# Performance work log

Hardware: AMD Instinct MI355X
Metric: run time of the kernel (lower is better)

Reference implementation:

```python
import jax, jax.numpy as jnp
import numpy as np

ROPE_DIM = 64       # config.rope_dim
GN_GROUPS = 32      # config.group_norm_num
GN_CHANNELS = 2048  # config.group_norm_channels == intermediate_size
GN_EPS = 1e-5


def rope_rotate(x):
    """lucidrains rotary-embedding-torch rotate_queries_or_keys:
    interleaved-pair rotation of the first ROPE_DIM features, rest pass through."""
    T = x.shape[-2]
    inv_freq = 1.0 / (10000.0 ** (jnp.arange(0, ROPE_DIM, 2, dtype=jnp.float32) / ROPE_DIM))
    freqs = jnp.arange(T, dtype=jnp.float32)[:, None] * inv_freq[None, :]  # (T, ROPE_DIM/2)
    freqs = jnp.repeat(freqs, 2, axis=-1)                                  # (T, ROPE_DIM)
    cos, sin = jnp.cos(freqs), jnp.sin(freqs)
    xr = x[..., :ROPE_DIM]
    x1, x2 = xr[..., 0::2], xr[..., 1::2]
    rot = jnp.stack((-x2, x1), axis=-1).reshape(xr.shape)  # rotate_half, interleaved
    xr = xr * cos + rot * sin
    return jnp.concatenate([xr, x[..., ROPE_DIM:]], axis=-1)


def group_norm_rows(x2d, weight, bias):
    """torch GroupNorm on a 2D (N, C) input: normalize each group of channels per row."""
    N, Cc = x2d.shape
    xg = x2d.reshape(N, GN_GROUPS, Cc // GN_GROUPS)
    mu = xg.mean(-1, keepdims=True)
    var = xg.var(-1, keepdims=True)
    xn = ((xg - mu) * jax.lax.rsqrt(var + GN_EPS)).reshape(N, Cc)
    return xn * weight + bias


def setup_inputs() -> dict:
    key = jax.random.key(0)
    ks = jax.random.split(key, 4)
    B, T, I, C = 2, 4096, 2048, 2048
    X = jax.random.normal(ks[0], (B, T, I), dtype=jnp.float32)
    S_n = jnp.zeros((B, C), dtype=jnp.float32)
    W_Q = jax.random.normal(ks[1], (I, C), dtype=jnp.float32) / I
    hh_b = jax.random.normal(ks[2], (C,), dtype=jnp.float32) * 0.02  # nn.Linear bias of self.hh
    gn_weight = jnp.ones((C,), dtype=jnp.float32)
    gn_bias = jnp.zeros((C,), dtype=jnp.float32)
    return {"X": X, "S_n": S_n, "W_Q": W_Q, "hh_b": hh_b,
            "gn_weight": gn_weight, "gn_bias": gn_bias}


def reference(X, S_n, W_Q, hh_b, gn_weight, gn_bias):
    # forward_auto_rec with chunk_len = T (single chunk, h_t starts at zeros):
    #   Q = ReLU(rope(X @ W_Q));  H = tanh(hh(0) + Q) = tanh(Q + b_hh)
    # K, V and the decay-masked A = (H K^T * D) V are computed in the source but
    # discarded (out = H), so they are dead code (DCE'd under jit) and omitted.
    B, T, _ = X.shape
    Q = jax.nn.relu(rope_rotate(X @ W_Q))   # (B, T, C)
    H = jnp.tanh(Q + hh_b)                  # (B, T, C)
    C = H.shape[-1]
    # dropout in eval mode = identity
    out = group_norm_rows(H.reshape(-1, C), gn_weight, gn_bias).reshape(B, T, C)
    # out.transpose(-2,-1).contiguous().view(B,T,C): reshape of the transposed layout
    out = jnp.swapaxes(out, -2, -1).reshape(B, T, C)
    return out, S_n
```

## Files before the change

kernel.cpp:

```cpp
#include <hip/hip_runtime.h>

#define T_DIM 4096
#define C_DIM 2048
#define K_DIM 2048

typedef __bf16 bf16x8 __attribute__((ext_vector_type(8)));
typedef float f32x4 __attribute__((ext_vector_type(4)));

__device__ __forceinline__ unsigned short f2bf(float f) {
  union { float f; unsigned int i; } x;
  x.f = f;
  unsigned int r = x.i + 0x7fffu + ((x.i >> 16) & 1u);
  return (unsigned short)(r >> 16);
}

#define GLD16(gsrc, ldst)                                                   \
  __builtin_amdgcn_global_load_lds(                                         \
      (const __attribute__((address_space(1))) unsigned int*)(gsrc),        \
      (__attribute__((address_space(3))) unsigned int*)(ldst), 16, 0, 0)

__global__ __launch_bounds__(256) void transpose_w(const float* __restrict__ W,
                                                   unsigned short* __restrict__ Wt) {
  __shared__ float tile[64][68];
  const int c0 = blockIdx.x * 64;
  const int r0 = blockIdx.y * 64;
  const int tid = threadIdx.x;
#pragma unroll
  for (int i = 0; i < 4; ++i) {
    int s = tid + i * 256;
    int r = s >> 4, c4 = (s & 15) * 4;
    *(float4*)&tile[r][c4] = *(const float4*)&W[(size_t)(r0 + r) * C_DIM + c0 + c4];
  }
  __syncthreads();
#pragma unroll
  for (int i = 0; i < 2; ++i) {
    int s = tid + i * 256;
    int n = s >> 3, k8 = (s & 7) * 8;
    __align__(16) unsigned short tmp[8];
#pragma unroll
    for (int j = 0; j < 8; ++j) tmp[j] = f2bf(tile[k8 + j][n]);
    *(uint4*)&Wt[(size_t)(c0 + n) * K_DIM + r0 + k8] = *(uint4*)tmp;
  }
}

__global__ __launch_bounds__(256) void cvt_x(const float* __restrict__ X,
                                             unsigned short* __restrict__ Xb) {
  size_t base = (size_t)blockIdx.x * 2048 + (size_t)threadIdx.x * 8;
  float4 a = *(const float4*)&X[base];
  float4 b = *(const float4*)&X[base + 4];
  __align__(16) unsigned short t[8];
  t[0] = f2bf(a.x); t[1] = f2bf(a.y); t[2] = f2bf(a.z); t[3] = f2bf(a.w);
  t[4] = f2bf(b.x); t[5] = f2bf(b.y); t[6] = f2bf(b.z); t[7] = f2bf(b.w);
  *(uint4*)&Xb[base] = *(const uint4*)t;
}

#define FOR_MN(OP) \
  OP(0,0) OP(0,1) OP(0,2) OP(0,3) \
  OP(1,0) OP(1,1) OP(1,2) OP(1,3) \
  OP(2,0) OP(2,1) OP(2,2) OP(2,3) \
  OP(3,0) OP(3,1) OP(3,2) OP(3,3)

#define DECL_ACC(m,n) f32x4 a##m##n = {0.f, 0.f, 0.f, 0.f};

template <bool ABF16>
__global__ __launch_bounds__(256, 2) void gemm_fused(const void* __restrict__ Av,
                                                     const unsigned short* __restrict__ Wt,
                                                     const float* __restrict__ hhb,
                                                     const float* __restrict__ gnw,
                                                     const float* __restrict__ gnb,
                                                     float* __restrict__ out) {
  constexpr int SMEM_BYTES = ABF16 ? 65536 : 49152;
  __shared__ __align__(16) char smem[SMEM_BYTES];
  unsigned short* lsA = (unsigned short*)smem;
  float* lsAf = (float*)smem;
  unsigned short* lsB = (unsigned short*)(smem + 32768);
  float(*lsO)[68] = (float(*)[68])smem;

  const int tid = threadIdx.x;
  const int wave = tid >> 6;
  const int lane = tid & 63;
  const int quad = lane >> 4;
  const int l16 = lane & 15;
  const int wm = wave >> 1, wn = wave & 1;

  const int bid = blockIdx.x;
  const int wg = (bid & 7) * 128 + (bid >> 3);
  const int m0 = (wg >> 4) * 128;
  const int n0 = (wg & 15) * 128;

  FOR_MN(DECL_ACC)

  if constexpr (ABF16) {
    const int srow = lane >> 3;
    const int scol = ((lane & 7) ^ (srow & 7)) * 8;
    const unsigned short* gA =
        (const unsigned short*)Av + (size_t)(m0 + wave * 32 + srow) * K_DIM + scol;
    const unsigned short* gB =
        Wt + (size_t)(n0 + wave * 32 + srow) * K_DIM + scol;

    const int xs0 = (quad * 8) ^ ((l16 & 7) << 3);
    const int xs1 = (32 + quad * 8) ^ ((l16 & 7) << 3);
    const int abase = (wm * 64 + l16) * 64;
    const int bbase = (wn * 64 + l16) * 64;

    auto stage = [&](int d, int koff) {
#pragma unroll
      for (int r = 0; r < 4; ++r)
        GLD16(gA + (size_t)(r * 8) * K_DIM + koff, lsA + d * 8192 + wave * 2048 + r * 512);
#pragma unroll
      for (int r = 0; r < 4; ++r)
        GLD16(gB + (size_t)(r * 8) * K_DIM + koff, lsB + d * 8192 + wave * 2048 + r * 512);
    };

    constexpr int NT = K_DIM / 64;
    stage(0, 0);
    for (int t = 0; t < NT; ++t) {
      const int cur = t & 1;
      if (t + 1 < NT) {
        stage(cur ^ 1, (t + 1) * 64);
        asm volatile("s_waitcnt vmcnt(8)" ::: "memory");
      } else {
        asm volatile("s_waitcnt vmcnt(0)" ::: "memory");
      }
      __builtin_amdgcn_s_barrier();
      asm volatile("" ::: "memory");

      const unsigned short* pa = lsA + cur * 8192;
      const unsigned short* pb = lsB + cur * 8192;

#define LOAD_AF16(m, XS) bf16x8 af##m = *(const bf16x8*)(const void*)(pa + abase + m * 1024 + XS);
#define LOAD_BF16(n, XS) bf16x8 bfr##n = *(const bf16x8*)(const void*)(pb + bbase + n * 1024 + XS);
#define MFMA_OP(m,n) \
      a##m##n = __builtin_amdgcn_mfma_f32_16x16x32_bf16(af##m, bfr##n, a##m##n, 0, 0, 0);
      {
        LOAD_AF16(0, xs0) LOAD_AF16(1, xs0) LOAD_AF16(2, xs0) LOAD_AF16(3, xs0)
        LOAD_BF16(0, xs0) LOAD_BF16(1, xs0) LOAD_BF16(2, xs0) LOAD_BF16(3, xs0)
        FOR_MN(MFMA_OP)
      }
      {
        LOAD_AF16(0, xs1) LOAD_AF16(1, xs1) LOAD_AF16(2, xs1) LOAD_AF16(3, xs1)
        LOAD_BF16(0, xs1) LOAD_BF16(1, xs1) LOAD_BF16(2, xs1) LOAD_BF16(3, xs1)
        FOR_MN(MFMA_OP)
      }
#undef LOAD_AF16
#undef LOAD_BF16

      asm volatile("s_waitcnt lgkmcnt(0)" ::: "memory");
      __builtin_amdgcn_sched_barrier(0);
      __builtin_amdgcn_s_barrier();
      asm volatile("" ::: "memory");
    }
  } else {
    const int srow32 = lane >> 3;
    const int scol32 = (((lane & 7) ^ srow32) * 4);
    const int srow16 = lane >> 2;
    const int scol16 = (((lane & 3) ^ (srow16 & 3)) * 8);
    const float* gA32 =
        (const float*)Av + (size_t)(m0 + wave * 32 + srow32) * K_DIM + scol32;
    const unsigned short* gB16 =
        Wt + (size_t)(n0 + wave * 32 + srow16) * K_DIM + scol16;

    const int axs = (quad ^ (l16 & 3)) * 8;
    const int bbase = (wn * 64 + l16) * 32 + axs;
    const int abasef = (wm * 64 + l16) * 32;
    const int u0 = ((2 * quad) ^ (l16 & 7)) * 4;
    const int u1 = ((2 * quad + 1) ^ (l16 & 7)) * 4;

    auto stage = [&](int d, int koff) {
      GLD16(gA32 + koff, lsAf + d * 4096 + wave * 1024);
      GLD16(gA32 + koff + 8 * K_DIM, lsAf + d * 4096 + wave * 1024 + 256);
      GLD16(gA32 + koff + 16 * K_DIM, lsAf + d * 4096 + wave * 1024 + 512);
      GLD16(gA32 + koff + 24 * K_DIM, lsAf + d * 4096 + wave * 1024 + 768);
      GLD16(gB16 + koff, lsB + d * 4096 + wave * 1024);
      GLD16(gB16 + koff + 16 * K_DIM, lsB + d * 4096 + wave * 1024 + 512);
    };

    constexpr int NT = K_DIM / 32;
    stage(0, 0);
    for (int t = 0; t < NT; ++t) {
      const int cur = t & 1;
      if (t + 1 < NT) {
        stage(cur ^ 1, (t + 1) * 32);
        asm volatile("s_waitcnt vmcnt(6)" ::: "memory");
      } else {
        asm volatile("s_waitcnt vmcnt(0)" ::: "memory");
      }
      __builtin_amdgcn_s_barrier();
      asm volatile("" ::: "memory");

      const float* paf = lsAf + cur * 4096;
      const unsigned short* pb = lsB + cur * 4096;

#define LOAD_AF32(m)                                                      \
      bf16x8 af##m;                                                       \
      { const float* ap_ = paf + abasef + m * 512;                        \
        f32x4 a0_ = *(const f32x4*)(ap_ + u0);                            \
        f32x4 a1_ = *(const f32x4*)(ap_ + u1);                            \
        af##m[0] = (__bf16)a0_[0]; af##m[1] = (__bf16)a0_[1];             \
        af##m[2] = (__bf16)a0_[2]; af##m[3] = (__bf16)a0_[3];             \
        af##m[4] = (__bf16)a1_[0]; af##m[5] = (__bf16)a1_[1];             \
        af##m[6] = (__bf16)a1_[2]; af##m[7] = (__bf16)a1_[3]; }
#define LOAD_BF32(n)                                                      \
      bf16x8 bfr##n = *(const bf16x8*)(const void*)(pb + bbase + n * 512);

      LOAD_AF32(0) LOAD_AF32(1) LOAD_AF32(2) LOAD_AF32(3)
      LOAD_BF32(0) LOAD_BF32(1) LOAD_BF32(2) LOAD_BF32(3)
      FOR_MN(MFMA_OP)
#undef LOAD_AF32
#undef LOAD_BF32

      asm volatile("s_waitcnt lgkmcnt(0)" ::: "memory");
      __builtin_amdgcn_sched_barrier(0);
      __builtin_amdgcn_s_barrier();
      asm volatile("" ::: "memory");
    }
  }

  const int c_base = n0 + wn * 64;
  const int t_base = (m0 & (T_DIM - 1)) + wm * 64;

#define LOADC(n)                                  \
  const int c##n = c_base + n * 16 + l16;         \
  const float hb##n = hhb[c##n];                  \
  const float gw##n = gnw[c##n];                  \
  const float gb##n = gnb[c##n];
  LOADC(0) LOADC(1) LOADC(2) LOADC(3)

  if (c_base == 0) {
#define ROPE_E(n,m,r)                                                   \
    { float v_ = a##m##n[r];                                            \
      float p_ = __shfl_xor(v_, 1, 64);                                 \
      int t_ = t_base + m * 16 + quad * 4 + r;                          \
      float ang_ = (float)t_ * fr_;                                     \
      float s_ = sinf(ang_);                                            \
      float co_ = cosf(ang_);                                           \
      a##m##n[r] = v_ * co_ + sg_ * p_ * s_; }
#define ROPE_M(n,m) ROPE_E(n,m,0) ROPE_E(n,m,1) ROPE_E(n,m,2) ROPE_E(n,m,3)
#define ROPE_N(n)                                                       \
    { int cc_ = n * 16 + l16;                                           \
      int ii_ = cc_ >> 1;                                               \
      float fr_ = expf(-(float)ii_ * 0.28782313662425572f);             \
      float sg_ = (cc_ & 1) ? 1.f : -1.f;                               \
      ROPE_M(n,0) ROPE_M(n,1) ROPE_M(n,2) ROPE_M(n,3) }
    ROPE_N(0) ROPE_N(1) ROPE_N(2) ROPE_N(3)
  }

#define GN_ROW(m,r)                                                     \
  { float h0_ = tanhf(fmaxf(a##m##0[r], 0.f) + hb0);                    \
    float h1_ = tanhf(fmaxf(a##m##1[r], 0.f) + hb1);                    \
    float h2_ = tanhf(fmaxf(a##m##2[r], 0.f) + hb2);                    \
    float h3_ = tanhf(fmaxf(a##m##3[r], 0.f) + hb3);                    \
    float s1_ = h0_ + h1_ + h2_ + h3_;                                  \
    float s2_ = h0_ * h0_ + h1_ * h1_ + h2_ * h2_ + h3_ * h3_;          \
    s1_ += __shfl_xor(s1_, 1, 64);  s2_ += __shfl_xor(s2_, 1, 64);      \
    s1_ += __shfl_xor(s1_, 2, 64);  s2_ += __shfl_xor(s2_, 2, 64);      \
    s1_ += __shfl_xor(s1_, 4, 64);  s2_ += __shfl_xor(s2_, 4, 64);      \
    s1_ += __shfl_xor(s1_, 8, 64);  s2_ += __shfl_xor(s2_, 8, 64);      \
    float mu_ = s1_ * 0.015625f;                                        \
    float var_ = s2_ * 0.015625f - mu_ * mu_;                           \
    float rs_ = rsqrtf(var_ + 1e-5f);                                   \
    a##m##0[r] = (h0_ - mu_) * rs_ * gw0 + gb0;                         \
    a##m##1[r] = (h1_ - mu_) * rs_ * gw1 + gb1;                         \
    a##m##2[r] = (h2_ - mu_) * rs_ * gw2 + gb2;                         \
    a##m##3[r] = (h3_ - mu_) * rs_ * gw3 + gb3; }
#define GN_M(m) GN_ROW(m,0) GN_ROW(m,1) GN_ROW(m,2) GN_ROW(m,3)
  GN_M(0) GN_M(1) GN_M(2) GN_M(3)

  const int bb = m0 >> 12;
  const int t0 = m0 & (T_DIM - 1);
#define ST_MN(m,n)                                                      \
  lsO[wn * 64 + n * 16 + l16][m * 16 + quad * 4 + 0] = a##m##n[0];      \
  lsO[wn * 64 + n * 16 + l16][m * 16 + quad * 4 + 1] = a##m##n[1];      \
  lsO[wn * 64 + n * 16 + l16][m * 16 + quad * 4 + 2] = a##m##n[2];      \
  lsO[wn * 64 + n * 16 + l16][m * 16 + quad * 4 + 3] = a##m##n[3];
#pragma unroll
  for (int h = 0; h < 2; ++h) {
    if (wm == h) {
      FOR_MN(ST_MN)
    }
    __syncthreads();
#pragma unroll
    for (int i = 0; i < 8; ++i) {
      int s = tid + i * 256;
      int cl = s >> 4;
      int t4 = (s & 15) * 4;
      float4 v = *(const float4*)&lsO[cl][t4];
      *(float4*)&out[(size_t)bb * C_DIM * T_DIM + (size_t)(n0 + cl) * T_DIM + t0 + h * 64 + t4] = v;
    }
    __syncthreads();
  }
}

__global__ __launch_bounds__(256) void copy_sn(const float* __restrict__ src,
                                               float* __restrict__ dst) {
  int i = blockIdx.x * 256 + threadIdx.x;
  dst[i] = src[i];
}

extern "C" void kernel_launch(void* const* d_in, const int* in_sizes, int n_in,
                              void* d_out, int out_size, void* d_ws, size_t ws_size,
                              hipStream_t stream) {
  const float* X = (const float*)d_in[0];
  const float* Sn = (const float*)d_in[1];
  const float* W = (const float*)d_in[2];
  const float* hhb = (const float*)d_in[3];
  const float* gnw = (const float*)d_in[4];
  const float* gnb = (const float*)d_in[5];
  float* out = (float*)d_out;

  unsigned short* Wt = (unsigned short*)d_ws;
  const size_t wt_bytes = (size_t)C_DIM * K_DIM * 2;
  const size_t xb_bytes = (size_t)2 * T_DIM * K_DIM * 2;

  transpose_w<<<dim3(32, 32), dim3(256), 0, stream>>>(W, Wt);

  if (ws_size >= wt_bytes + xb_bytes) {
    unsigned short* Xb = Wt + (size_t)C_DIM * K_DIM;
    cvt_x<<<dim3(8192), dim3(256), 0, stream>>>(X, Xb);
    gemm_fused<true><<<dim3(1024), dim3(256), 0, stream>>>(Xb, Wt, hhb, gnw, gnb, out);
  } else {
    gemm_fused<false><<<dim3(1024), dim3(256), 0, stream>>>(X, Wt, hhb, gnw, gnb, out);
  }

  copy_sn<<<dim3(16), dim3(256), 0, stream>>>(Sn, out + (size_t)16777216);
}
```

Baseline: 295.6 us.

## Shrink bf16 GEMM K-tile to 32 and raise occupancy to four blocks per CU

The bf16-A GEMM path now stages 32-wide K tiles instead of 64-wide ones. This roughly halves its LDS footprint, and launch bounds are raised from 2 to 4 blocks per CU so more waves can hide latency. The LDS swizzle is changed to a new XOR pattern that avoids bank conflicts with 32-element rows, and the fp32-A path adopts the same B swizzle. In exchange there are twice as many barrier-synchronised iterations, each issuing fewer MFMAs, and the tighter register cap may cause spills.

```diff
diff --git a/kernel.cpp b/kernel.cpp
--- a/kernel.cpp
+++ b/kernel.cpp
@@ -62,18 +62,21 @@
 
 #define DECL_ACC(m,n) f32x4 a##m##n = {0.f, 0.f, 0.f, 0.f};
 
+#define MFMA_OP(m,n) \
+  a##m##n = __builtin_amdgcn_mfma_f32_16x16x32_bf16(af##m, bfr##n, a##m##n, 0, 0, 0);
+
 template <bool ABF16>
-__global__ __launch_bounds__(256, 2) void gemm_fused(const void* __restrict__ Av,
+__global__ __launch_bounds__(256, 4) void gemm_fused(const void* __restrict__ Av,
                                                      const unsigned short* __restrict__ Wt,
                                                      const float* __restrict__ hhb,
                                                      const float* __restrict__ gnw,
                                                      const float* __restrict__ gnb,
                                                      float* __restrict__ out) {
-  constexpr int SMEM_BYTES = ABF16 ? 65536 : 49152;
+  constexpr int SMEM_BYTES = ABF16 ? 34816 : 49152;
   __shared__ __align__(16) char smem[SMEM_BYTES];
   unsigned short* lsA = (unsigned short*)smem;
   float* lsAf = (float*)smem;
-  unsigned short* lsB = (unsigned short*)(smem + 32768);
+  unsigned short* lsB = (unsigned short*)(smem + (ABF16 ? 16384 : 32768));
   float(*lsO)[68] = (float(*)[68])smem;
 
   const int tid = threadIdx.x;
@@ -91,57 +94,45 @@
   FOR_MN(DECL_ACC)
 
   if constexpr (ABF16) {
-    const int srow = lane >> 3;
-    const int scol = ((lane & 7) ^ (srow & 7)) * 8;
+    const int srow = lane >> 2;
+    const int scol = ((lane & 3) ^ ((lane >> 3) & 3)) * 8;
     const unsigned short* gA =
         (const unsigned short*)Av + (size_t)(m0 + wave * 32 + srow) * K_DIM + scol;
     const unsigned short* gB =
         Wt + (size_t)(n0 + wave * 32 + srow) * K_DIM + scol;
 
-    const int xs0 = (quad * 8) ^ ((l16 & 7) << 3);
-    const int xs1 = (32 + quad * 8) ^ ((l16 & 7) << 3);
-    const int abase = (wm * 64 + l16) * 64;
-    const int bbase = (wn * 64 + l16) * 64;
+    const int axs = (quad ^ ((l16 >> 1) & 3)) * 8;
+    const int abase = (wm * 64 + l16) * 32;
+    const int bbase = (wn * 64 + l16) * 32;
 
     auto stage = [&](int d, int koff) {
-#pragma unroll
-      for (int r = 0; r < 4; ++r)
-        GLD16(gA + (size_t)(r * 8) * K_DIM + koff, lsA + d * 8192 + wave * 2048 + r * 512);
-#pragma unroll
-      for (int r = 0; r < 4; ++r)
-        GLD16(gB + (size_t)(r * 8) * K_DIM + koff, lsB + d * 8192 + wave * 2048 + r * 512);
+      GLD16(gA + koff, lsA + d * 4096 + wave * 1024);
+      GLD16(gA + (size_t)16 * K_DIM + koff, lsA + d * 4096 + wave * 1024 + 512);
+      GLD16(gB + koff, lsB + d * 4096 + wave * 1024);
+      GLD16(gB + (size_t)16 * K_DIM + koff, lsB + d * 4096 + wave * 1024 + 512);
     };
 
-    constexpr int NT = K_DIM / 64;
+    constexpr int NT = K_DIM / 32;
     stage(0, 0);
     for (int t = 0; t < NT; ++t) {
       const int cur = t & 1;
       if (t + 1 < NT) {
-        stage(cur ^ 1, (t + 1) * 64);
-        asm volatile("s_waitcnt vmcnt(8)" ::: "memory");
+        stage(cur ^ 1, (t + 1) * 32);
+        asm volatile("s_waitcnt vmcnt(4)" ::: "memory");
       } else {
         asm volatile("s_waitcnt vmcnt(0)" ::: "memory");
       }
       __builtin_amdgcn_s_barrier();
       asm volatile("" ::: "memory");
 
-      const unsigned short* pa = lsA + cur * 8192;
-      const unsigned short* pb = lsB + cur * 8192;
-
-#define LOAD_AF16(m, XS) bf16x8 af##m = *(const bf16x8*)(const void*)(pa + abase + m * 1024 + XS);
-#define LOAD_BF16(n, XS) bf16x8 bfr##n = *(const bf16x8*)(const void*)(pb + bbase + n * 1024 + XS);
-#define MFMA_OP(m,n) \
-      a##m##n = __builtin_amdgcn_mfma_f32_16x16x32_bf16(af##m, bfr##n, a##m##n, 0, 0, 0);
-      {
-        LOAD_AF16(0, xs0) LOAD_AF16(1, xs0) LOAD_AF16(2, xs0) LOAD_AF16(3, xs0)
-        LOAD_BF16(0, xs0) LOAD_BF16(1, xs0) LOAD_BF16(2, xs0) LOAD_BF16(3, xs0)
-        FOR_MN(MFMA_OP)
-      }
-      {
-        LOAD_AF16(0, xs1) LOAD_AF16(1, xs1) LOAD_AF16(2, xs1) LOAD_AF16(3, xs1)
-        LOAD_BF16(0, xs1) LOAD_BF16(1, xs1) LOAD_BF16(2, xs1) LOAD_BF16(3, xs1)
-        FOR_MN(MFMA_OP)
-      }
+      const unsigned short* pa = lsA + cur * 4096;
+      const unsigned short* pb = lsB + cur * 4096;
+
+#define LOAD_AF16(m) bf16x8 af##m = *(const bf16x8*)(const void*)(pa + abase + m * 512 + axs);
+#define LOAD_BF16(n) bf16x8 bfr##n = *(const bf16x8*)(const void*)(pb + bbase + n * 512 + axs);
+      LOAD_AF16(0) LOAD_AF16(1) LOAD_AF16(2) LOAD_AF16(3)
+      LOAD_BF16(0) LOAD_BF16(1) LOAD_BF16(2) LOAD_BF16(3)
+      FOR_MN(MFMA_OP)
 #undef LOAD_AF16
 #undef LOAD_BF16
 
@@ -154,14 +145,14 @@
     const int srow32 = lane >> 3;
     const int scol32 = (((lane & 7) ^ srow32) * 4);
     const int srow16 = lane >> 2;
-    const int scol16 = (((lane & 3) ^ (srow16 & 3)) * 8);
+    const int scol16 = ((lane & 3) ^ ((lane >> 3) & 3)) * 8;
     const float* gA32 =
         (const float*)Av + (size_t)(m0 + wave * 32 + srow32) * K_DIM + scol32;
     const unsigned short* gB16 =
         Wt + (size_t)(n0 + wave * 32 + srow16) * K_DIM + scol16;
 
-    const int axs = (quad ^ (l16 & 3)) * 8;
-    const int bbase = (wn * 64 + l16) * 32 + axs;
+    const int bxs = (quad ^ ((l16 >> 1) & 3)) * 8;
+    const int bbase = (wn * 64 + l16) * 32;
     const int abasef = (wm * 64 + l16) * 32;
     const int u0 = ((2 * quad) ^ (l16 & 7)) * 4;
     const int u1 = ((2 * quad + 1) ^ (l16 & 7)) * 4;
@@ -172,7 +163,7 @@
       GLD16(gA32 + koff + 16 * K_DIM, lsAf + d * 4096 + wave * 1024 + 512);
       GLD16(gA32 + koff + 24 * K_DIM, lsAf + d * 4096 + wave * 1024 + 768);
       GLD16(gB16 + koff, lsB + d * 4096 + wave * 1024);
-      GLD16(gB16 + koff + 16 * K_DIM, lsB + d * 4096 + wave * 1024 + 512);
+      GLD16(gB16 + (size_t)16 * K_DIM + koff, lsB + d * 4096 + wave * 1024 + 512);
     };
 
     constexpr int NT = K_DIM / 32;
@@ -201,7 +192,7 @@
         af##m[4] = (__bf16)a1_[0]; af##m[5] = (__bf16)a1_[1];             \
         af##m[6] = (__bf16)a1_[2]; af##m[7] = (__bf16)a1_[3]; }
 #define LOAD_BF32(n)                                                      \
-      bf16x8 bfr##n = *(const bf16x8*)(const void*)(pb + bbase + n * 512);
+      bf16x8 bfr##n = *(const bf16x8*)(const void*)(pb + bbase + n * 512 + bxs);
 
       LOAD_AF32(0) LOAD_AF32(1) LOAD_AF32(2) LOAD_AF32(3)
       LOAD_BF32(0) LOAD_BF32(1) LOAD_BF32(2) LOAD_BF32(3)
```

Measured after the change: 410.9 us. +39.0%, slower.

## Use 256x256 block tile with 8 waves for the bf16 fused GEMM path

Applied to the files above, without the earlier changes.

Replaces the 128x128 bf16 GEMM kernel with a 256x256 tile kernel that runs 512 threads in a 2x4 wave grid, each wave holding 8x4 MFMA accumulators. It uses 128KB of LDS for double buffering. The goal is to cut global and LDS traffic per FLOP and reach higher MFMA intensity, at the cost of fewer blocks (256), which is roughly one per CU, and much higher register pressure. The fp32 fallback kernel is split into its own function and gets a modified B-tile swizzle.

```diff
diff --git a/kernel.cpp b/kernel.cpp
--- a/kernel.cpp
+++ b/kernel.cpp
@@ -54,179 +54,15 @@
   *(uint4*)&Xb[base] = *(const uint4*)t;
 }
 
-#define FOR_MN(OP) \
-  OP(0,0) OP(0,1) OP(0,2) OP(0,3) \
-  OP(1,0) OP(1,1) OP(1,2) OP(1,3) \
-  OP(2,0) OP(2,1) OP(2,2) OP(2,3) \
-  OP(3,0) OP(3,1) OP(3,2) OP(3,3)
-
-#define DECL_ACC(m,n) f32x4 a##m##n = {0.f, 0.f, 0.f, 0.f};
-
-template <bool ABF16>
-__global__ __launch_bounds__(256, 2) void gemm_fused(const void* __restrict__ Av,
-                                                     const unsigned short* __restrict__ Wt,
-                                                     const float* __restrict__ hhb,
-                                                     const float* __restrict__ gnw,
-                                                     const float* __restrict__ gnb,
-                                                     float* __restrict__ out) {
-  constexpr int SMEM_BYTES = ABF16 ? 65536 : 49152;
-  __shared__ __align__(16) char smem[SMEM_BYTES];
-  unsigned short* lsA = (unsigned short*)smem;
-  float* lsAf = (float*)smem;
-  unsigned short* lsB = (unsigned short*)(smem + 32768);
-  float(*lsO)[68] = (float(*)[68])smem;
-
-  const int tid = threadIdx.x;
-  const int wave = tid >> 6;
-  const int lane = tid & 63;
-  const int quad = lane >> 4;
-  const int l16 = lane & 15;
-  const int wm = wave >> 1, wn = wave & 1;
-
-  const int bid = blockIdx.x;
-  const int wg = (bid & 7) * 128 + (bid >> 3);
-  const int m0 = (wg >> 4) * 128;
-  const int n0 = (wg & 15) * 128;
-
-  FOR_MN(DECL_ACC)
-
-  if constexpr (ABF16) {
-    const int srow = lane >> 3;
-    const int scol = ((lane & 7) ^ (srow & 7)) * 8;
-    const unsigned short* gA =
-        (const unsigned short*)Av + (size_t)(m0 + wave * 32 + srow) * K_DIM + scol;
-    const unsigned short* gB =
-        Wt + (size_t)(n0 + wave * 32 + srow) * K_DIM + scol;
-
-    const int xs0 = (quad * 8) ^ ((l16 & 7) << 3);
-    const int xs1 = (32 + quad * 8) ^ ((l16 & 7) << 3);
-    const int abase = (wm * 64 + l16) * 64;
-    const int bbase = (wn * 64 + l16) * 64;
-
-    auto stage = [&](int d, int koff) {
-#pragma unroll
-      for (int r = 0; r < 4; ++r)
-        GLD16(gA + (size_t)(r * 8) * K_DIM + koff, lsA + d * 8192 + wave * 2048 + r * 512);
-#pragma unroll
-      for (int r = 0; r < 4; ++r)
-        GLD16(gB + (size_t)(r * 8) * K_DIM + koff, lsB + d * 8192 + wave * 2048 + r * 512);
-    };
-
-    constexpr int NT = K_DIM / 64;
-    stage(0, 0);
-    for (int t = 0; t < NT; ++t) {
-      const int cur = t & 1;
-      if (t + 1 < NT) {
-        stage(cur ^ 1, (t + 1) * 64);
-        asm volatile("s_waitcnt vmcnt(8)" ::: "memory");
-      } else {
-        asm volatile("s_waitcnt vmcnt(0)" ::: "memory");
-      }
-      __builtin_amdgcn_s_barrier();
-      asm volatile("" ::: "memory");
-
-      const unsigned short* pa = lsA + cur * 8192;
-      const unsigned short* pb = lsB + cur * 8192;
-
-#define LOAD_AF16(m, XS) bf16x8 af##m = *(const bf16x8*)(const void*)(pa + abase + m * 1024 + XS);
-#define LOAD_BF16(n, XS) bf16x8 bfr##n = *(const bf16x8*)(const void*)(pb + bbase + n * 1024 + XS);
 #define MFMA_OP(m,n) \
-      a##m##n = __builtin_amdgcn_mfma_f32_16x16x32_bf16(af##m, bfr##n, a##m##n, 0, 0, 0);
-      {
-        LOAD_AF16(0, xs0) LOAD_AF16(1, xs0) LOAD_AF16(2, xs0) LOAD_AF16(3, xs0)
-        LOAD_BF16(0, xs0) LOAD_BF16(1, xs0) LOAD_BF16(2, xs0) LOAD_BF16(3, xs0)
-        FOR_MN(MFMA_OP)
-      }
-      {
-        LOAD_AF16(0, xs1) LOAD_AF16(1, xs1) LOAD_AF16(2, xs1) LOAD_AF16(3, xs1)
-        LOAD_BF16(0, xs1) LOAD_BF16(1, xs1) LOAD_BF16(2, xs1) LOAD_BF16(3, xs1)
-        FOR_MN(MFMA_OP)
-      }
-#undef LOAD_AF16
-#undef LOAD_BF16
-
-      asm volatile("s_waitcnt lgkmcnt(0)" ::: "memory");
-      __builtin_amdgcn_sched_barrier(0);
-      __builtin_amdgcn_s_barrier();
-      asm volatile("" ::: "memory");
-    }
-  } else {
-    const int srow32 = lane >> 3;
-    const int scol32 = (((lane & 7) ^ srow32) * 4);
-    const int srow16 = lane >> 2;
-    const int scol16 = (((lane & 3) ^ (srow16 & 3)) * 8);
-    const float* gA32 =
-        (const float*)Av + (size_t)(m0 + wave * 32 + srow32) * K_DIM + scol32;
-    const unsigned short* gB16 =
-        Wt + (size_t)(n0 + wave * 32 + srow16) * K_DIM + scol16;
-
-    const int axs = (quad ^ (l16 & 3)) * 8;
-    const int bbase = (wn * 64 + l16) * 32 + axs;
-    const int abasef = (wm * 64 + l16) * 32;
-    const int u0 = ((2 * quad) ^ (l16 & 7)) * 4;
-    const int u1 = ((2 * quad + 1) ^ (l16 & 7)) * 4;
-
-    auto stage = [&](int d, int koff) {
-      GLD16(gA32 + koff, lsAf + d * 4096 + wave * 1024);
-      GLD16(gA32 + koff + 8 * K_DIM, lsAf + d * 4096 + wave * 1024 + 256);
-      GLD16(gA32 + koff + 16 * K_DIM, lsAf + d * 4096 + wave * 1024 + 512);
-      GLD16(gA32 + koff + 24 * K_DIM, lsAf + d * 4096 + wave * 1024 + 768);
-      GLD16(gB16 + koff, lsB + d * 4096 + wave * 1024);
-      GLD16(gB16 + koff + 16 * K_DIM, lsB + d * 4096 + wave * 1024 + 512);
-    };
-
-    constexpr int NT = K_DIM / 32;
-    stage(0, 0);
-    for (int t = 0; t < NT; ++t) {
-      const int cur = t & 1;
-      if (t + 1 < NT) {
-        stage(cur ^ 1, (t + 1) * 32);
-        asm volatile("s_waitcnt vmcnt(6)" ::: "memory");
-      } else {
-        asm volatile("s_waitcnt vmcnt(0)" ::: "memory");
-      }
-      __builtin_amdgcn_s_barrier();
-      asm volatile("" ::: "memory");
-
-      const float* paf = lsAf + cur * 4096;
-      const unsigned short* pb = lsB + cur * 4096;
-
-#define LOAD_AF32(m)                                                      \
-      bf16x8 af##m;                                                       \
-      { const float* ap_ = paf + abasef + m * 512;                        \
-        f32x4 a0_ = *(const f32x4*)(ap_ + u0);                            \
-        f32x4 a1_ = *(const f32x4*)(ap_ + u1);                            \
-        af##m[0] = (__bf16)a0_[0]; af##m[1] = (__bf16)a0_[1];             \
-        af##m[2] = (__bf16)a0_[2]; af##m[3] = (__bf16)a0_[3];             \
-        af##m[4] = (__bf16)a1_[0]; af##m[5] = (__bf16)a1_[1];             \
-        af##m[6] = (__bf16)a1_[2]; af##m[7] = (__bf16)a1_[3]; }
-#define LOAD_BF32(n)                                                      \
-      bf16x8 bfr##n = *(const bf16x8*)(const void*)(pb + bbase + n * 512);
-
-      LOAD_AF32(0) LOAD_AF32(1) LOAD_AF32(2) LOAD_AF32(3)
-      LOAD_BF32(0) LOAD_BF32(1) LOAD_BF32(2) LOAD_BF32(3)
-      FOR_MN(MFMA_OP)
-#undef LOAD_AF32
-#undef LOAD_BF32
-
-      asm volatile("s_waitcnt lgkmcnt(0)" ::: "memory");
-      __builtin_amdgcn_sched_barrier(0);
-      __builtin_amdgcn_s_barrier();
-      asm volatile("" ::: "memory");
-    }
-  }
-
-  const int c_base = n0 + wn * 64;
-  const int t_base = (m0 & (T_DIM - 1)) + wm * 64;
+  a##m##n = __builtin_amdgcn_mfma_f32_16x16x32_bf16(af##m, bfr##n, a##m##n, 0, 0, 0);
 
 #define LOADC(n)                                  \
   const int c##n = c_base + n * 16 + l16;         \
   const float hb##n = hhb[c##n];                  \
   const float gw##n = gnw[c##n];                  \
   const float gb##n = gnb[c##n];
-  LOADC(0) LOADC(1) LOADC(2) LOADC(3)
-
-  if (c_base == 0) {
+
 #define ROPE_E(n,m,r)                                                   \
     { float v_ = a##m##n[r];                                            \
       float p_ = __shfl_xor(v_, 1, 64);                                 \
@@ -236,14 +72,6 @@
       float co_ = cosf(ang_);                                           \
       a##m##n[r] = v_ * co_ + sg_ * p_ * s_; }
 #define ROPE_M(n,m) ROPE_E(n,m,0) ROPE_E(n,m,1) ROPE_E(n,m,2) ROPE_E(n,m,3)
-#define ROPE_N(n)                                                       \
-    { int cc_ = n * 16 + l16;                                           \
-      int ii_ = cc_ >> 1;                                               \
-      float fr_ = expf(-(float)ii_ * 0.28782313662425572f);             \
-      float sg_ = (cc_ & 1) ? 1.f : -1.f;                               \
-      ROPE_M(n,0) ROPE_M(n,1) ROPE_M(n,2) ROPE_M(n,3) }
-    ROPE_N(0) ROPE_N(1) ROPE_N(2) ROPE_N(3)
-  }
 
 #define GN_ROW(m,r)                                                     \
   { float h0_ = tanhf(fmaxf(a##m##0[r], 0.f) + hb0);                    \
@@ -264,6 +92,254 @@
     a##m##2[r] = (h2_ - mu_) * rs_ * gw2 + gb2;                         \
     a##m##3[r] = (h3_ - mu_) * rs_ * gw3 + gb3; }
 #define GN_M(m) GN_ROW(m,0) GN_ROW(m,1) GN_ROW(m,2) GN_ROW(m,3)
+
+#define FOR_MN8(OP) \
+  OP(0,0) OP(0,1) OP(0,2) OP(0,3) OP(1,0) OP(1,1) OP(1,2) OP(1,3) \
+  OP(2,0) OP(2,1) OP(2,2) OP(2,3) OP(3,0) OP(3,1) OP(3,2) OP(3,3) \
+  OP(4,0) OP(4,1) OP(4,2) OP(4,3) OP(5,0) OP(5,1) OP(5,2) OP(5,3) \
+  OP(6,0) OP(6,1) OP(6,2) OP(6,3) OP(7,0) OP(7,1) OP(7,2) OP(7,3)
+#define DECL_ACC8(m,n) f32x4 a##m##n = {0.f, 0.f, 0.f, 0.f};
+
+__global__ __launch_bounds__(512, 2) void gemm_fused256(const unsigned short* __restrict__ Xb,
+                                                        const unsigned short* __restrict__ Wt,
+                                                        const float* __restrict__ hhb,
+                                                        const float* __restrict__ gnw,
+                                                        const float* __restrict__ gnb,
+                                                        float* __restrict__ out) {
+  __shared__ __align__(16) char smem[131072];
+  unsigned short* lsA = (unsigned short*)smem;
+  unsigned short* lsB = (unsigned short*)(smem + 65536);
+  float(*lsO)[68] = (float(*)[68])smem;
+
+  const int tid = threadIdx.x;
+  const int wave = tid >> 6;
+  const int lane = tid & 63;
+  const int quad = lane >> 4;
+  const int l16 = lane & 15;
+  const int wm = wave >> 2, wn = wave & 3;
+
+  const int bid = blockIdx.x;
+  const int wg = (bid & 7) * 32 + (bid >> 3);
+  const int n0 = (wg >> 5) * 256;
+  const int m0 = (wg & 31) * 256;
+
+  FOR_MN8(DECL_ACC8)
+
+  const int srow = lane >> 3;
+  const int scol = ((lane & 7) ^ (srow & 7)) * 8;
+  const unsigned short* gA = Xb + (size_t)(m0 + wave * 32 + srow) * K_DIM + scol;
+  const unsigned short* gB = Wt + (size_t)(n0 + wave * 32 + srow) * K_DIM + scol;
+
+  const int xs0 = (quad * 8) ^ ((l16 & 7) << 3);
+  const int xs1 = (32 + quad * 8) ^ ((l16 & 7) << 3);
+  const int abase = (wm * 128 + l16) * 64;
+  const int bbase = (wn * 64 + l16) * 64;
+
+  auto stage = [&](int d, int koff) {
+#pragma unroll
+    for (int r = 0; r < 4; ++r)
+      GLD16(gA + (size_t)(r * 8) * K_DIM + koff, lsA + d * 16384 + wave * 2048 + r * 512);
+#pragma unroll
+    for (int r = 0; r < 4; ++r)
+      GLD16(gB + (size_t)(r * 8) * K_DIM + koff, lsB + d * 16384 + wave * 2048 + r * 512);
+  };
+
+  constexpr int NT = K_DIM / 64;
+  stage(0, 0);
+  for (int t = 0; t < NT; ++t) {
+    const int cur = t & 1;
+    if (t + 1 < NT) {
+      stage(cur ^ 1, (t + 1) * 64);
+      asm volatile("s_waitcnt vmcnt(8)" ::: "memory");
+    } else {
+      asm volatile("s_waitcnt vmcnt(0)" ::: "memory");
+    }
+    __builtin_amdgcn_s_barrier();
+    asm volatile("" ::: "memory");
+
+    const unsigned short* pa = lsA + cur * 16384;
+    const unsigned short* pb = lsB + cur * 16384;
+
+#define LOAD_AF8(m, XS) bf16x8 af##m = *(const bf16x8*)(const void*)(pa + abase + m * 1024 + XS);
+#define LOAD_BF8(n, XS) bf16x8 bfr##n = *(const bf16x8*)(const void*)(pb + bbase + n * 1024 + XS);
+    {
+      LOAD_AF8(0, xs0) LOAD_AF8(1, xs0) LOAD_AF8(2, xs0) LOAD_AF8(3, xs0)
+      LOAD_AF8(4, xs0) LOAD_AF8(5, xs0) LOAD_AF8(6, xs0) LOAD_AF8(7, xs0)
+      LOAD_BF8(0, xs0) LOAD_BF8(1, xs0) LOAD_BF8(2, xs0) LOAD_BF8(3, xs0)
+      FOR_MN8(MFMA_OP)
+    }
+    {
+      LOAD_AF8(0, xs1) LOAD_AF8(1, xs1) LOAD_AF8(2, xs1) LOAD_AF8(3, xs1)
+      LOAD_AF8(4, xs1) LOAD_AF8(5, xs1) LOAD_AF8(6, xs1) LOAD_AF8(7, xs1)
+      LOAD_BF8(0, xs1) LOAD_BF8(1, xs1) LOAD_BF8(2, xs1) LOAD_BF8(3, xs1)
+      FOR_MN8(MFMA_OP)
+    }
+#undef LOAD_AF8
+#undef LOAD_BF8
+
+    asm volatile("s_waitcnt lgkmcnt(0)" ::: "memory");
+    __builtin_amdgcn_sched_barrier(0);
+    __builtin_amdgcn_s_barrier();
+    asm volatile("" ::: "memory");
+  }
+
+  const int c_base = n0 + wn * 64;
+  const int t_base = (m0 & (T_DIM - 1)) + wm * 128;
+
+  LOADC(0) LOADC(1) LOADC(2) LOADC(3)
+
+  if (c_base == 0) {
+#define ROPE_N8(n)                                                      \
+    { int cc_ = n * 16 + l16;                                           \
+      int ii_ = cc_ >> 1;                                               \
+      float fr_ = expf(-(float)ii_ * 0.28782313662425572f);             \
+      float sg_ = (cc_ & 1) ? 1.f : -1.f;                               \
+      ROPE_M(n,0) ROPE_M(n,1) ROPE_M(n,2) ROPE_M(n,3)                   \
+      ROPE_M(n,4) ROPE_M(n,5) ROPE_M(n,6) ROPE_M(n,7) }
+    ROPE_N8(0) ROPE_N8(1) ROPE_N8(2) ROPE_N8(3)
+  }
+
+  GN_M(0) GN_M(1) GN_M(2) GN_M(3) GN_M(4) GN_M(5) GN_M(6) GN_M(7)
+
+  const int bb = m0 >> 12;
+  const int t0 = m0 & (T_DIM - 1);
+#define ST1R(m,ml,n)                                                     \
+  lsO[wn * 64 + n * 16 + l16][ml * 16 + quad * 4 + 0] = a##m##n[0];      \
+  lsO[wn * 64 + n * 16 + l16][ml * 16 + quad * 4 + 1] = a##m##n[1];      \
+  lsO[wn * 64 + n * 16 + l16][ml * 16 + quad * 4 + 2] = a##m##n[2];      \
+  lsO[wn * 64 + n * 16 + l16][ml * 16 + quad * 4 + 3] = a##m##n[3];
+#define ST_ROW(m,ml) ST1R(m,ml,0) ST1R(m,ml,1) ST1R(m,ml,2) ST1R(m,ml,3)
+#pragma unroll
+  for (int h = 0; h < 4; ++h) {
+    if (wm == (h >> 1)) {
+      if ((h & 1) == 0) {
+        ST_ROW(0,0) ST_ROW(1,1) ST_ROW(2,2) ST_ROW(3,3)
+      } else {
+        ST_ROW(4,0) ST_ROW(5,1) ST_ROW(6,2) ST_ROW(7,3)
+      }
+    }
+    __syncthreads();
+#pragma unroll
+    for (int i = 0; i < 8; ++i) {
+      int s = tid + i * 512;
+      int cl = s >> 4;
+      int t4 = (s & 15) * 4;
+      float4 v = *(const float4*)&lsO[cl][t4];
+      *(float4*)&out[(size_t)bb * C_DIM * T_DIM + (size_t)(n0 + cl) * T_DIM + t0 + h * 64 + t4] = v;
+    }
+    __syncthreads();
+  }
+}
+
+#define FOR_MN(OP) \
+  OP(0,0) OP(0,1) OP(0,2) OP(0,3) \
+  OP(1,0) OP(1,1) OP(1,2) OP(1,3) \
+  OP(2,0) OP(2,1) OP(2,2) OP(2,3) \
+  OP(3,0) OP(3,1) OP(3,2) OP(3,3)
+#define DECL_ACC(m,n) f32x4 a##m##n = {0.f, 0.f, 0.f, 0.f};
+
+__global__ __launch_bounds__(256, 2) void gemm_fused_f32(const float* __restrict__ Av,
+                                                         const unsigned short* __restrict__ Wt,
+                                                         const float* __restrict__ hhb,
+                                                         const float* __restrict__ gnw,
+                                                         const float* __restrict__ gnb,
+                                                         float* __restrict__ out) {
+  __shared__ __align__(16) char smem[49152];
+  float* lsAf = (float*)smem;
+  unsigned short* lsB = (unsigned short*)(smem + 32768);
+  float(*lsO)[68] = (float(*)[68])smem;
+
+  const int tid = threadIdx.x;
+  const int wave = tid >> 6;
+  const int lane = tid & 63;
+  const int quad = lane >> 4;
+  const int l16 = lane & 15;
+  const int wm = wave >> 1, wn = wave & 1;
+
+  const int bid = blockIdx.x;
+  const int wg = (bid & 7) * 128 + (bid >> 3);
+  const int m0 = (wg >> 4) * 128;
+  const int n0 = (wg & 15) * 128;
+
+  FOR_MN(DECL_ACC)
+
+  const int srow32 = lane >> 3;
+  const int scol32 = (((lane & 7) ^ srow32) * 4);
+  const int srow16 = lane >> 2;
+  const int scol16 = ((lane & 3) ^ ((lane >> 3) & 3)) * 8;
+  const float* gA32 = Av + (size_t)(m0 + wave * 32 + srow32) * K_DIM + scol32;
+  const unsigned short* gB16 = Wt + (size_t)(n0 + wave * 32 + srow16) * K_DIM + scol16;
+
+  const int bxs = (quad ^ ((l16 >> 1) & 3)) * 8;
+  const int bbase = (wn * 64 + l16) * 32;
+  const int abasef = (wm * 64 + l16) * 32;
+  const int u0 = ((2 * quad) ^ (l16 & 7)) * 4;
+  const int u1 = ((2 * quad + 1) ^ (l16 & 7)) * 4;
+
+  auto stage = [&](int d, int koff) {
+    GLD16(gA32 + koff, lsAf + d * 4096 + wave * 1024);
+    GLD16(gA32 + koff + 8 * K_DIM, lsAf + d * 4096 + wave * 1024 + 256);
+    GLD16(gA32 + koff + 16 * K_DIM, lsAf + d * 4096 + wave * 1024 + 512);
+    GLD16(gA32 + koff + 24 * K_DIM, lsAf + d * 4096 + wave * 1024 + 768);
+    GLD16(gB16 + koff, lsB + d * 4096 + wave * 1024);
+    GLD16(gB16 + (size_t)16 * K_DIM + koff, lsB + d * 4096 + wave * 1024 + 512);
+  };
+
+  constexpr int NT = K_DIM / 32;
+  stage(0, 0);
+  for (int t = 0; t < NT; ++t) {
+    const int cur = t & 1;
+    if (t + 1 < NT) {
+      stage(cur ^ 1, (t + 1) * 32);
+      asm volatile("s_waitcnt vmcnt(6)" ::: "memory");
+    } else {
+      asm volatile("s_waitcnt vmcnt(0)" ::: "memory");
+    }
+    __builtin_amdgcn_s_barrier();
+    asm volatile("" ::: "memory");
+
+    const float* paf = lsAf + cur * 4096;
+    const unsigned short* pb = lsB + cur * 4096;
+
+#define LOAD_AF32(m)                                                      \
+    bf16x8 af##m;                                                         \
+    { const float* ap_ = paf + abasef + m * 512;                          \
+      f32x4 a0_ = *(const f32x4*)(ap_ + u0);                              \
+      f32x4 a1_ = *(const f32x4*)(ap_ + u1);                              \
+      af##m[0] = (__bf16)a0_[0]; af##m[1] = (__bf16)a0_[1];               \
+      af##m[2] = (__bf16)a0_[2]; af##m[3] = (__bf16)a0_[3];               \
+      af##m[4] = (__bf16)a1_[0]; af##m[5] = (__bf16)a1_[1];               \
+      af##m[6] = (__bf16)a1_[2]; af##m[7] = (__bf16)a1_[3]; }
+#define LOAD_BF32(n)                                                      \
+    bf16x8 bfr##n = *(const bf16x8*)(const void*)(pb + bbase + n * 512 + bxs);
+
+    LOAD_AF32(0) LOAD_AF32(1) LOAD_AF32(2) LOAD_AF32(3)
+    LOAD_BF32(0) LOAD_BF32(1) LOAD_BF32(2) LOAD_BF32(3)
+    FOR_MN(MFMA_OP)
+#undef LOAD_AF32
+#undef LOAD_BF32
+
+    asm volatile("s_waitcnt lgkmcnt(0)" ::: "memory");
+    __builtin_amdgcn_sched_barrier(0);
+    __builtin_amdgcn_s_barrier();
+    asm volatile("" ::: "memory");
+  }
+
+  const int c_base = n0 + wn * 64;
+  const int t_base = (m0 & (T_DIM - 1)) + wm * 64;
+
+  LOADC(0) LOADC(1) LOADC(2) LOADC(3)
+
+  if (c_base == 0) {
+#define ROPE_N(n)                                                       \
+    { int cc_ = n * 16 + l16;                                           \
+      int ii_ = cc_ >> 1;                                               \
+      float fr_ = expf(-(float)ii_ * 0.28782313662425572f);             \
+      float sg_ = (cc_ & 1) ? 1.f : -1.f;                                \
+      ROPE_M(n,0) ROPE_M(n,1) ROPE_M(n,2) ROPE_M(n,3) }
+    ROPE_N(0) ROPE_N(1) ROPE_N(2) ROPE_N(3)
+  }
+
   GN_M(0) GN_M(1) GN_M(2) GN_M(3)
 
   const int bb = m0 >> 12;
@@ -317,9 +393,9 @@
   if (ws_size >= wt_bytes + xb_bytes) {
     unsigned short* Xb = Wt + (size_t)C_DIM * K_DIM;
     cvt_x<<<dim3(8192), dim3(256), 0, stream>>>(X, Xb);
-    gemm_fused<true><<<dim3(1024), dim3(256), 0, stream>>>(Xb, Wt, hhb, gnw, gnb, out);
+    gemm_fused256<<<dim3(256), dim3(512), 0, stream>>>(Xb, Wt, hhb, gnw, gnb, out);
   } else {
-    gemm_fused<false><<<dim3(1024), dim3(256), 0, stream>>>(X, Wt, hhb, gnw, gnb, out);
+    gemm_fused_f32<<<dim3(1024), dim3(256), 0, stream>>>(X, Wt, hhb, gnw, gnb, out);
   }
 
   copy_sn<<<dim3(16), dim3(256), 0, stream>>>(Sn, out + (size_t)16777216);
```

After: 435.1 us. 47.2% more time.
